# Optimization experiments

Measured on AMD Instinct MI355X. Metric: run time of the kernel, lower is better.

Reference implementation:

```python
import jax, jax.numpy as jnp
import numpy as np

N, NFEAT, NHID, NCLASS, NLAYERS = 4096, 512, 512, 40, 3
NEG = -9e15


def _adj(key, p=0.01):
    # sparse binary adjacency with self-loops, matching the `adj > 0` masking
    a = (jax.random.uniform(key, (N, N)) < p).astype(jnp.float32)
    return jnp.minimum(a + jnp.eye(N, dtype=jnp.float32), 1.0)


def setup_inputs() -> dict:
    key = jax.random.key(0)
    ks = jax.random.split(key, 16)
    inp = {
        "x": jax.random.normal(ks[0], (N, NFEAT), jnp.float32),
        "adj_att": _adj(ks[1]),
        "adj1": _adj(ks[2]),
        "adj2": _adj(ks[3]),
        "hop_select": jnp.ones((NLAYERS,), jnp.float32),
    }
    s1 = 1.0 / np.sqrt(NFEAT)
    s2 = 1.0 / np.sqrt(NHID)
    for i in range(NLAYERS):
        inp[f"W_fc{i}"] = jax.random.uniform(ks[4 + i], (NFEAT, NHID), jnp.float32, -s1, s1)
        inp[f"b_fc{i}"] = jnp.zeros((NHID,), jnp.float32)
    for i in range(NLAYERS - 1):
        inp[f"W_q{i}"] = jax.random.uniform(ks[7 + 2 * i], (NHID, NHID), jnp.float32, -s2, s2)
        inp[f"b_q{i}"] = jnp.zeros((NHID,), jnp.float32)
        inp[f"W_k{i}"] = jax.random.uniform(ks[8 + 2 * i], (NHID, NHID), jnp.float32, -s2, s2)
        inp[f"b_k{i}"] = jnp.zeros((NHID,), jnp.float32)
    s3 = 1.0 / np.sqrt(NHID * NLAYERS)
    inp["W_cls"] = jax.random.uniform(ks[11], (NHID * NLAYERS, NCLASS), jnp.float32, -s3, s3)
    inp["b_cls"] = jnp.zeros((NCLASS,), jnp.float32)
    return inp


def _gatv3_forward(x, adj_att, adj1, adj2, hop_select,
                   W_fc0, b_fc0, W_fc1, b_fc1, W_fc2, b_fc2,
                   W_q0, b_q0, W_k0, b_k0, W_q1, b_q1, W_k1, b_k1,
                   W_cls, b_cls):
    mask = jax.nn.softmax(hop_select, axis=-1)
    adjs = [None, adj1, adj2]
    fc = [(W_fc0, b_fc0), (W_fc1, b_fc1), (W_fc2, b_fc2)]
    qk = [(W_q0, b_q0, W_k0, b_k0), (W_q1, b_q1, W_k1, b_k1)]
    outs = []
    tmp_1 = None
    for i in range(NLAYERS):
        W, b = fc[i]
        tmp = x @ W + b  # [N, nhid]
        if adjs[i] is not None:
            adj = adjs[i]
            Wq, bq, Wk, bk = qk[i - 1]
            t_att = adj_att @ tmp                      # [N, nhid]
            Q = adj_att @ (t_att @ Wq + bq)            # GCN1 Q, act=None
            K = adj_att @ (t_att @ Wk + bk)            # GCN1 K, act=None
            scores = jnp.where(adj > 0, Q @ K.T, NEG)  # masked QK^T
            att = jax.nn.softmax(scores, axis=-1)
            tmp_1 = jnp.where(adj > 0, att, 0.0)
            tmp = att @ tmp
        # F.normalize(p=2, dim=1) with eps=1e-12 clamp
        nrm = jnp.maximum(jnp.sqrt(jnp.sum(tmp * tmp, axis=1, keepdims=True)), 1e-12)
        outs.append(mask[i] * (tmp / nrm))
    final = jnp.concatenate(outs, axis=1)          # [N, 3*nhid]
    out = jax.nn.relu(final)                       # dropout is identity in eval
    logits = out @ W_cls + b_cls
    return jax.nn.log_softmax(logits, axis=1), tmp_1


def reference(x, adj_att, adj1, adj2, hop_select,
              W_fc0, b_fc0, W_fc1, b_fc1, W_fc2, b_fc2,
              W_q0, b_q0, W_k0, b_k0, W_q1, b_q1, W_k1, b_k1,
              W_cls, b_cls):
    return _gatv3_forward(x, adj_att, adj1, adj2, hop_select,
                          W_fc0, b_fc0, W_fc1, b_fc1, W_fc2, b_fc2,
                          W_q0, b_q0, W_k0, b_k0, W_q1, b_q1, W_k1, b_k1,
                          W_cls, b_cls)
```

## Files before the change

kernel.cpp:

```cpp
#include <hip/hip_runtime.h>
#include <math.h>

#define NN 4096
#define DD 512
#define ELL 128

typedef unsigned long long u64;
typedef __attribute__((ext_vector_type(8))) short short8;
typedef __attribute__((ext_vector_type(8))) unsigned short ushort8;
typedef __attribute__((ext_vector_type(4))) float f32x4;

static __device__ __forceinline__ unsigned short f2bf(float f) {
  unsigned u = __float_as_uint(f);
  unsigned r = (u + 0x7fffu + ((u >> 16) & 1u)) >> 16;
  return (unsigned short)r;
}
static __device__ __forceinline__ float bf2f(unsigned short h) {
  return __uint_as_float(((unsigned)h) << 16);
}

struct Build3 {
  const float *adj0, *adj1, *adj2;
  int *c0, *c1, *c2;
  int *n0, *n1, *n2;
};

__global__ __launch_bounds__(256) void k_build3(Build3 p) {
  const int s = blockIdx.y;
  const float* adj = s == 0 ? p.adj0 : (s == 1 ? p.adj1 : p.adj2);
  int* cols = s == 0 ? p.c0 : (s == 1 ? p.c1 : p.c2);
  int* cnt  = s == 0 ? p.n0 : (s == 1 ? p.n1 : p.n2);
  const int wv = threadIdx.x >> 6;
  const int lane = threadIdx.x & 63;
  const int r = blockIdx.x * 4 + wv;
  const float* row = adj + (size_t)r * NN;
  int* rc = cols + (size_t)r * ELL;
  int base = 0;
  for (int c0 = 0; c0 < NN; c0 += 256) {
    float4 v = *(const float4*)(row + c0 + lane * 4);
    u64 m0 = __ballot(v.x > 0.f);
    u64 m1 = __ballot(v.y > 0.f);
    u64 m2 = __ballot(v.z > 0.f);
    u64 m3 = __ballot(v.w > 0.f);
    u64 below = (1ull << lane) - 1ull;
    int pre = base + __popcll(m0 & below) + __popcll(m1 & below) +
              __popcll(m2 & below) + __popcll(m3 & below);
    int own = 0;
    const int cb = c0 + 4 * lane;
    if (v.x > 0.f) { int id = pre + own; if (id < ELL) rc[id] = cb + 0; own++; }
    if (v.y > 0.f) { int id = pre + own; if (id < ELL) rc[id] = cb + 1; own++; }
    if (v.z > 0.f) { int id = pre + own; if (id < ELL) rc[id] = cb + 2; own++; }
    if (v.w > 0.f) { int id = pre + own; if (id < ELL) rc[id] = cb + 3; own++; }
    base += __popcll(m0) + __popcll(m1) + __popcll(m2) + __popcll(m3);
  }
  if (lane == 0) cnt[r] = base < ELL ? base : ELL;
}

struct SplitE { const float* src; unsigned short* dst; int rows; int bstyle; };
struct Split4 { SplitE e[4]; };

__global__ __launch_bounds__(256) void k_split(Split4 p) {
  SplitE e = p.e[blockIdx.y];
  if (!e.src) return;
  const int oct = blockIdx.x * 256 + threadIdx.x;
  if (oct >= e.rows * 64) return;
  float v[8];
  size_t toff;
  if (!e.bstyle) {
    const int m = oct >> 6, kg = oct & 63;
    const float* sp = e.src + (size_t)m * 512 + kg * 8;
    float4 u0 = *(const float4*)sp;
    float4 u1 = *(const float4*)(sp + 4);
    v[0] = u0.x; v[1] = u0.y; v[2] = u0.z; v[3] = u0.w;
    v[4] = u1.x; v[5] = u1.y; v[6] = u1.z; v[7] = u1.w;
    toff = ((size_t)(m >> 7) * 16 + (kg >> 2)) * 4096 +
           (size_t)((m & 127) >> 4) * 512 + (size_t)(kg & 3) * 128 +
           (size_t)(m & 15) * 8;
  } else {
    const int n = oct & 511, kog = oct >> 9;
    const int k0 = kog * 8;
#pragma unroll
    for (int i = 0; i < 8; i++) v[i] = e.src[(size_t)(k0 + i) * 512 + n];
    toff = ((size_t)(n >> 7) * 16 + (kog >> 2)) * 4096 +
           (size_t)((n & 127) >> 4) * 512 + (size_t)(kog & 3) * 128 +
           (size_t)(n & 15) * 8;
  }
  ushort8 h0, h1, h2;
#pragma unroll
  for (int i = 0; i < 8; i++) {
    float f = v[i];
    unsigned short a0 = f2bf(f);
    float r1 = f - bf2f(a0);
    unsigned short a1 = f2bf(r1);
    float r2 = r1 - bf2f(a1);
    unsigned short a2 = f2bf(r2);
    h0[i] = a0; h1[i] = a1; h2[i] = a2;
  }
  const size_t stride = (size_t)e.rows * 512;
  *(ushort8*)(e.dst + toff) = h0;
  *(ushort8*)(e.dst + stride + toff) = h1;
  *(ushort8*)(e.dst + 2 * stride + toff) = h2;
}

struct ToBf {
  const float *s0, *s1;
  unsigned short *d0, *d1;
};

__global__ __launch_bounds__(256) void k_tobf16(ToBf p) {
  const float* s = blockIdx.y ? p.s1 : p.s0;
  unsigned short* d = blockIdx.y ? p.d1 : p.d0;
  const size_t i = ((size_t)blockIdx.x * 256 + threadIdx.x) * 8;
  float4 a = *(const float4*)(s + i);
  float4 b = *(const float4*)(s + i + 4);
  ushort8 h;
  h[0] = f2bf(a.x); h[1] = f2bf(a.y); h[2] = f2bf(a.z); h[3] = f2bf(a.w);
  h[4] = f2bf(b.x); h[5] = f2bf(b.y); h[6] = f2bf(b.z); h[7] = f2bf(b.w);
  *(ushort8*)(d + i) = h;
}

struct GmP {
  const unsigned short *A0, *A1, *A2;
  const unsigned short *B0, *B1, *B2;
  const float *b0, *b1, *b2;
  float *C0, *C1, *C2;
  size_t sA, sB;
};

#define MMTERM(sa)                                                          \
  _Pragma("unroll")                                                         \
  for (int mi = 0; mi < 4; mi++) {                                          \
    _Pragma("unroll")                                                       \
    for (int ni = 0; ni < 4; ni++)                                          \
      acc[mi][ni] = __builtin_amdgcn_mfma_f32_16x16x32_bf16(                \
          af[sa][mi], bf[ni], acc[mi][ni], 0, 0, 0);                        \
  }

__global__ __launch_bounds__(256) void k_gemm_mfma(GmP p) {
  __shared__ __align__(16) unsigned short Al[3][4096];
  __shared__ __align__(16) unsigned short Bl[3][4096];
  const int tid = threadIdx.x;
  const int mat = blockIdx.y >> 2;
  const int nb = blockIdx.y & 3;
  const int mb = blockIdx.x;
  const unsigned short* A = mat == 0 ? p.A0 : (mat == 1 ? p.A1 : p.A2);
  const unsigned short* B = mat == 0 ? p.B0 : (mat == 1 ? p.B1 : p.B2);
  const float* bias = mat == 0 ? p.b0 : (mat == 1 ? p.b1 : p.b2);
  float* C = mat == 0 ? p.C0 : (mat == 1 ? p.C1 : p.C2);
  const int lane = tid & 63, w = tid >> 6, wr = w >> 1, wc = w & 1;
  const size_t s8A = p.sA >> 3, s8B = p.sB >> 3;

  f32x4 acc[4][4];
#pragma unroll
  for (int mi = 0; mi < 4; mi++)
#pragma unroll
    for (int ni = 0; ni < 4; ni++) acc[mi][ni] = (f32x4){0.f, 0.f, 0.f, 0.f};

  for (int kb = 0; kb < 16; kb++) {
    const short8* ga = (const short8*)(A + ((size_t)mb * 16 + kb) * 4096);
    const short8* gb = (const short8*)(B + ((size_t)nb * 16 + kb) * 4096);
    __syncthreads();
#pragma unroll
    for (int s = 0; s < 3; s++) {
#pragma unroll
      for (int c = 0; c < 2; c++) {
        const int o = tid + c * 256;
        ((short8*)Al[s])[o] = ga[(size_t)s * s8A + o];
        ((short8*)Bl[s])[o] = gb[(size_t)s * s8B + o];
      }
    }
    __syncthreads();
    short8 af[3][4];
#pragma unroll
    for (int s = 0; s < 3; s++)
#pragma unroll
      for (int mi = 0; mi < 4; mi++)
        af[s][mi] = ((const short8*)Al[s])[(wr * 4 + mi) * 64 + lane];
    short8 bf[4];
#pragma unroll
    for (int ni = 0; ni < 4; ni++)
      bf[ni] = ((const short8*)Bl[0])[(wc * 4 + ni) * 64 + lane];
    MMTERM(0) MMTERM(1) MMTERM(2)
#pragma unroll
    for (int ni = 0; ni < 4; ni++)
      bf[ni] = ((const short8*)Bl[1])[(wc * 4 + ni) * 64 + lane];
    MMTERM(0) MMTERM(1)
#pragma unroll
    for (int ni = 0; ni < 4; ni++)
      bf[ni] = ((const short8*)Bl[2])[(wc * 4 + ni) * 64 + lane];
    MMTERM(0)
  }

  const int m0 = mb * 128 + wr * 64;
  const int n0c = nb * 128 + wc * 64 + (lane & 15);
  const int r0 = (lane >> 4) * 4;
#pragma unroll
  for (int mi = 0; mi < 4; mi++) {
#pragma unroll
    for (int ni = 0; ni < 4; ni++) {
      const int col = n0c + ni * 16;
      const float bb = bias ? bias[col] : 0.f;
      f32x4 a = acc[mi][ni];
#pragma unroll
      for (int r = 0; r < 4; r++)
        C[(size_t)(m0 + mi * 16 + r0 + r) * DD + col] = a[r] + bb;
    }
  }
}

struct GemmNT {
  const float *A0, *B0, *A1, *B1;
  float *C0, *C1;
};

__global__ __launch_bounds__(256) void k_gemm_nt(GemmNT p) {
  __shared__ __align__(16) float As[32][68];
  __shared__ __align__(16) float Bs[32][68];
  const int tid = threadIdx.x;
  const int mat = blockIdx.y >> 3;
  const int n0 = (blockIdx.y & 7) * 64;
  const int m0 = blockIdx.x * 64;
  const float* A = mat == 0 ? p.A0 : p.A1;
  const float* B = mat == 0 ? p.B0 : p.B1;
  float* C       = mat == 0 ? p.C0 : p.C1;
  const int tx = tid & 15, ty = tid >> 4;
  const int lr = tid >> 3, lc = (tid & 7) * 4;

  float4 fa[2], fb[2];
#pragma unroll
  for (int q = 0; q < 2; q++) {
    fa[q] = *(const float4*)(A + (size_t)(m0 + lr + 32 * q) * DD + lc);
    fb[q] = *(const float4*)(B + (size_t)(n0 + lr + 32 * q) * DD + lc);
  }
#pragma unroll
  for (int q = 0; q < 2; q++) {
    As[lc + 0][lr + 32 * q] = fa[q].x;
    As[lc + 1][lr + 32 * q] = fa[q].y;
    As[lc + 2][lr + 32 * q] = fa[q].z;
    As[lc + 3][lr + 32 * q] = fa[q].w;
    Bs[lc + 0][lr + 32 * q] = fb[q].x;
    Bs[lc + 1][lr + 32 * q] = fb[q].y;
    Bs[lc + 2][lr + 32 * q] = fb[q].z;
    Bs[lc + 3][lr + 32 * q] = fb[q].w;
  }
  __syncthreads();

  float acc[4][4];
#pragma unroll
  for (int i = 0; i < 4; i++)
#pragma unroll
    for (int j = 0; j < 4; j++) acc[i][j] = 0.f;

  for (int t = 0; t < 16; t++) {
    if (t < 15) {
      const int k0 = (t + 1) * 32;
#pragma unroll
      for (int q = 0; q < 2; q++) {
        fa[q] = *(const float4*)(A + (size_t)(m0 + lr + 32 * q) * DD + k0 + lc);
        fb[q] = *(const float4*)(B + (size_t)(n0 + lr + 32 * q) * DD + k0 + lc);
      }
    }
#pragma unroll
    for (int kk = 0; kk < 32; kk++) {
      float4 a = *(const float4*)&As[kk][ty * 4];
      float4 b = *(const float4*)&Bs[kk][tx * 4];
      float av[4] = {a.x, a.y, a.z, a.w};
      float bv[4] = {b.x, b.y, b.z, b.w};
#pragma unroll
      for (int i = 0; i < 4; i++)
#pragma unroll
        for (int j = 0; j < 4; j++) acc[i][j] = fmaf(av[i], bv[j], acc[i][j]);
    }
    __syncthreads();
    if (t < 15) {
#pragma unroll
      for (int q = 0; q < 2; q++) {
        As[lc + 0][lr + 32 * q] = fa[q].x;
        As[lc + 1][lr + 32 * q] = fa[q].y;
        As[lc + 2][lr + 32 * q] = fa[q].z;
        As[lc + 3][lr + 32 * q] = fa[q].w;
        Bs[lc + 0][lr + 32 * q] = fb[q].x;
        Bs[lc + 1][lr + 32 * q] = fb[q].y;
        Bs[lc + 2][lr + 32 * q] = fb[q].z;
        Bs[lc + 3][lr + 32 * q] = fb[q].w;
      }
      __syncthreads();
    }
  }

#pragma unroll
  for (int i = 0; i < 4; i++) {
    const int m = m0 + ty * 4 + i;
    float4 o = {acc[i][0], acc[i][1], acc[i][2], acc[i][3]};
    *(float4*)(C + (size_t)m * DD + n0 + tx * 4) = o;
  }
}

struct W12P {
  const float *Wq0, *bk0, *Wk0, *bq0;
  const float *Wq1, *bk1, *Wk1, *bq1;
  float *w10, *w20, *w11, *w21, *gam;
};

__global__ __launch_bounds__(256) void k_w12(W12P p) {
  const int l = blockIdx.y;
  const float* Wq = l ? p.Wq1 : p.Wq0;
  const float* bk = l ? p.bk1 : p.bk0;
  const float* Wk = l ? p.Wk1 : p.Wk0;
  const float* bq = l ? p.bq1 : p.bq0;
  float* w1 = l ? p.w11 : p.w10;
  float* w2 = l ? p.w21 : p.w20;
  const int wv = threadIdx.x >> 6, lane = threadIdx.x & 63;
  const int r = blockIdx.x * 4 + wv;
  float s1 = 0.f, s2 = 0.f;
  for (int k = lane; k < DD; k += 64) {
    s1 = fmaf(Wq[(size_t)r * DD + k], bk[k], s1);
    s2 = fmaf(Wk[(size_t)r * DD + k], bq[k], s2);
  }
#pragma unroll
  for (int off = 32; off > 0; off >>= 1) {
    s1 += __shfl_xor(s1, off);
    s2 += __shfl_xor(s2, off);
  }
  if (lane == 0) { w1[r] = s1; w2[r] = s2; }
  if (blockIdx.x == 0 && wv == 0) {
    float g = 0.f;
    for (int k = lane; k < DD; k += 64) g = fmaf(bq[k], bk[k], g);
#pragma unroll
    for (int off = 32; off > 0; off >>= 1) g += __shfl_xor(g, off);
    if (lane == 0) p.gam[l] = g;
  }
}

struct AbP {
  const float *U1, *U2, *w10, *w20, *w11, *w21;
  float *a1, *b1, *a2, *b2;
};

__global__ __launch_bounds__(256) void k_ab(AbP p) {
  const int wv = threadIdx.x >> 6, lane = threadIdx.x & 63;
  const int r = blockIdx.x * 4 + wv;
  const int base = lane * 8;
  float4 wa0 = *(const float4*)(p.w10 + base);
  float4 wa1 = *(const float4*)(p.w10 + base + 4);
  float4 wb0 = *(const float4*)(p.w20 + base);
  float4 wb1 = *(const float4*)(p.w20 + base + 4);
  float4 u0 = *(const float4*)(p.U1 + (size_t)r * DD + base);
  float4 u1 = *(const float4*)(p.U1 + (size_t)r * DD + base + 4);
  float sa = u0.x * wa0.x + u0.y * wa0.y + u0.z * wa0.z + u0.w * wa0.w +
             u1.x * wa1.x + u1.y * wa1.y + u1.z * wa1.z + u1.w * wa1.w;
  float sb = u0.x * wb0.x + u0.y * wb0.y + u0.z * wb0.z + u0.w * wb0.w +
             u1.x * wb1.x + u1.y * wb1.y + u1.z * wb1.z + u1.w * wb1.w;
#pragma unroll
  for (int off = 32; off > 0; off >>= 1) {
    sa += __shfl_xor(sa, off);
    sb += __shfl_xor(sb, off);
  }
  if (lane == 0) { p.a1[r] = sa; p.b1[r] = sb; }
  wa0 = *(const float4*)(p.w11 + base);
  wa1 = *(const float4*)(p.w11 + base + 4);
  wb0 = *(const float4*)(p.w21 + base);
  wb1 = *(const float4*)(p.w21 + base + 4);
  u0 = *(const float4*)(p.U2 + (size_t)r * DD + base);
  u1 = *(const float4*)(p.U2 + (size_t)r * DD + base + 4);
  sa = u0.x * wa0.x + u0.y * wa0.y + u0.z * wa0.z + u0.w * wa0.w +
       u1.x * wa1.x + u1.y * wa1.y + u1.z * wa1.z + u1.w * wa1.w;
  sb = u0.x * wb0.x + u0.y * wb0.y + u0.z * wb0.z + u0.w * wb0.w +
       u1.x * wb1.x + u1.y * wb1.y + u1.z * wb1.z + u1.w * wb1.w;
#pragma unroll
  for (int off = 32; off > 0; off >>= 1) {
    sa += __shfl_xor(sa, off);
    sb += __shfl_xor(sb, off);
  }
  if (lane == 0) { p.a2[r] = sa; p.b2[r] = sb; }
}

struct Sd2 {
  const int *cols0, *cnts0, *cols1, *cnts1;
  const float *V0, *U0, *al0, *be0;
  const unsigned short *T0;
  const float *V1, *U1, *al1, *be1;
  const unsigned short *T1;
  const float* gam;
  const int* degA;
  float *out0, *out1, *dense;
};

__global__ __launch_bounds__(256) void k_sddmm_out(Sd2 p) {
  const int l = blockIdx.y;
  const int* cols = l ? p.cols1 : p.cols0;
  const int* cnts = l ? p.cnts1 : p.cnts0;
  const float* V = l ? p.V1 : p.V0;
  const float* U = l ? p.U1 : p.U0;
  const float* al = l ? p.al1 : p.al0;
  const float* be = l ? p.be1 : p.be0;
  const unsigned short* Tb = l ? p.T1 : p.T0;
  float* out = l ? p.out1 : p.out0;
  float* dense = l ? p.dense : nullptr;
  const int r = blockIdx.x;
  const int t = threadIdx.x;
  const int lane = t & 63, wv = t >> 6;
  const int cnt = cnts[r];
  __shared__ int scol[ELL];
  __shared__ float ssc[ELL];
  if (t < ELL) scol[t] = (t < cnt) ? cols[(size_t)r * ELL + t] : 0;
  if (dense) {
    float4 z = {0.f, 0.f, 0.f, 0.f};
    float4* drow = (float4*)(dense + (size_t)r * NN);
#pragma unroll
    for (int q = 0; q < 4; q++) drow[t + 256 * q] = z;
  }
  __syncthreads();
  const float g = p.gam[l];
  const float dr = (float)p.degA[r];
  const float ar = al[r];
  const float* Vr = V + (size_t)r * DD + lane * 8;
  float4 q0 = *(const float4*)Vr;
  float4 q1 = *(const float4*)(Vr + 4);
  for (int k = wv; k < cnt; k += 4) {
    const int c = scol[k];
    const float* Uc = U + (size_t)c * DD + lane * 8;
    float4 k0 = *(const float4*)Uc;
    float4 k1 = *(const float4*)(Uc + 4);
    float s = q0.x * k0.x + q0.y * k0.y + q0.z * k0.z + q0.w * k0.w +
              q1.x * k1.x + q1.y * k1.y + q1.z * k1.z + q1.w * k1.w;
#pragma unroll
    for (int off = 32; off > 0; off >>= 1) s += __shfl_xor(s, off);
    if (lane == 0) {
      const float dc = (float)p.degA[c];
      ssc[k] = s + dc * ar + dr * be[c] + dr * dc * g;
    }
  }
  __syncthreads();
  if (wv == 0) {
    float v0 = (lane < cnt) ? ssc[lane] : -INFINITY;
    float v1 = (lane + 64 < cnt) ? ssc[lane + 64] : -INFINITY;
    float mx = fmaxf(v0, v1);
#pragma unroll
    for (int off = 32; off > 0; off >>= 1) mx = fmaxf(mx, __shfl_xor(mx, off));
    float e0 = (lane < cnt) ? expf(v0 - mx) : 0.f;
    float e1 = (lane + 64 < cnt) ? expf(v1 - mx) : 0.f;
    float sm = e0 + e1;
#pragma unroll
    for (int off = 32; off > 0; off >>= 1) sm += __shfl_xor(sm, off);
    float inv = 1.f / sm;
    if (lane < cnt) ssc[lane] = e0 * inv;
    if (lane + 64 < cnt) ssc[lane + 64] = e1 * inv;
  }
  __syncthreads();
  if (t < cnt && dense) dense[(size_t)r * NN + scol[t]] = ssc[t];
  float a0 = 0.f, a1 = 0.f;
#pragma unroll 4
  for (int k = 0; k < cnt; k++) {
    const float v = ssc[k];
    const unsigned u = *(const unsigned*)(Tb + (size_t)scol[k] * DD + t * 2);
    a0 = fmaf(v, __uint_as_float(u << 16), a0);
    a1 = fmaf(v, __uint_as_float(u & 0xffff0000u), a1);
  }
  float2 o = {a0, a1};
  *(float2*)(out + (size_t)r * DD + t * 2) = o;
}

struct SpF {
  const int *colsA, *cntsA, *colsB, *cntsB;
  const float *BA, *BB;
  float *CA, *CB;
};

__global__ __launch_bounds__(256) void k_spmm_f4(SpF p) {
  const int mat = blockIdx.y;
  const int* cols = mat ? p.colsB : p.colsA;
  const int* cnts = mat ? p.cntsB : p.cntsA;
  const float* B = mat ? p.BB : p.BA;
  float* C = mat ? p.CB : p.CA;
  const int hr = threadIdx.x >> 7;
  const int j = threadIdx.x & 127;
  const int row = blockIdx.x * 2 + hr;
  __shared__ int scol[2][ELL];
  const int cnt = cnts[row];
  scol[hr][j] = (j < cnt) ? cols[(size_t)row * ELL + j] : 0;
  __syncthreads();
  float4 acc = {0.f, 0.f, 0.f, 0.f};
#pragma unroll 4
  for (int k = 0; k < cnt; k++) {
    float4 b = *(const float4*)(B + (size_t)scol[hr][k] * DD + j * 4);
    acc.x += b.x; acc.y += b.y; acc.z += b.z; acc.w += b.w;
  }
  *(float4*)(C + (size_t)row * DD + j * 4) = acc;
}

__global__ __launch_bounds__(256) void k_norm_cls(const float* __restrict__ T0,
                                                  const float* __restrict__ T1,
                                                  const float* __restrict__ T2,
                                                  const float* __restrict__ hop,
                                                  const float* __restrict__ Wc,
                                                  const float* __restrict__ bc,
                                                  float* __restrict__ out) {
  const int r = blockIdx.x;
  const int t = threadIdx.x;
  const int lane = t & 63, wv = t >> 6;
  __shared__ __align__(16) float srow[1536];
  __shared__ float red[4];
  __shared__ float pr[6][40];
  float h0 = hop[0], h1 = hop[1], h2 = hop[2];
  float hm = fmaxf(h0, fmaxf(h1, h2));
  float e0 = expf(h0 - hm), e1 = expf(h1 - hm), e2 = expf(h2 - hm);
  float minv = 1.f / (e0 + e1 + e2);
  float mask[3] = {e0 * minv, e1 * minv, e2 * minv};
  const float* Ts[3] = {T0, T1, T2};
#pragma unroll
  for (int s = 0; s < 3; s++) {
    float x0 = Ts[s][(size_t)r * DD + t];
    float x1 = Ts[s][(size_t)r * DD + t + 256];
    float ss = x0 * x0 + x1 * x1;
#pragma unroll
    for (int off = 32; off > 0; off >>= 1) ss += __shfl_xor(ss, off);
    if (lane == 0) red[wv] = ss;
    __syncthreads();
    float tot = red[0] + red[1] + red[2] + red[3];
    float nrm = fmaxf(sqrtf(tot), 1e-12f);
    float sc = mask[s] / nrm;
    srow[s * DD + t] = fmaxf(x0 * sc, 0.f);
    srow[s * DD + t + 256] = fmaxf(x1 * sc, 0.f);
    __syncthreads();
  }
  float part = 0.f;
  const int col = t % 40, seg = t / 40;
  if (seg < 6) {
    const float* w = Wc + col;
#pragma unroll 4
    for (int k = seg * 256; k < seg * 256 + 256; k++)
      part = fmaf(srow[k], w[(size_t)k * 40], part);
    pr[seg][col] = part;
  }
  __syncthreads();
  if (t < 64) {
    float lg = -INFINITY;
    if (t < 40) {
      lg = bc[t];
#pragma unroll
      for (int s6 = 0; s6 < 6; s6++) lg += pr[s6][t];
    }
    float mx = lg;
#pragma unroll
    for (int off = 32; off > 0; off >>= 1) mx = fmaxf(mx, __shfl_xor(mx, off));
    float ex = (t < 40) ? expf(lg - mx) : 0.f;
    float sm = ex;
#pragma unroll
    for (int off = 32; off > 0; off >>= 1) sm += __shfl_xor(sm, off);
    float ls = logf(sm);
    if (t < 40) out[(size_t)r * 40 + t] = lg - mx - ls;
  }
}

extern "C" void kernel_launch(void* const* d_in, const int* in_sizes, int n_in,
                              void* d_out, int out_size, void* d_ws, size_t ws_size,
                              hipStream_t stream) {
  (void)in_sizes; (void)n_in; (void)out_size; (void)ws_size;
  const float* x    = (const float*)d_in[0];
  const float* adjA = (const float*)d_in[1];
  const float* adj1 = (const float*)d_in[2];
  const float* adj2 = (const float*)d_in[3];
  const float* hop  = (const float*)d_in[4];
  const float* Wfc0 = (const float*)d_in[5];  const float* bfc0 = (const float*)d_in[6];
  const float* Wfc1 = (const float*)d_in[7];  const float* bfc1 = (const float*)d_in[8];
  const float* Wfc2 = (const float*)d_in[9];  const float* bfc2 = (const float*)d_in[10];
  const float* Wq0  = (const float*)d_in[11]; const float* bq0  = (const float*)d_in[12];
  const float* Wk0  = (const float*)d_in[13]; const float* bk0  = (const float*)d_in[14];
  const float* Wq1  = (const float*)d_in[15]; const float* bq1  = (const float*)d_in[16];
  const float* Wk1  = (const float*)d_in[17]; const float* bk1  = (const float*)d_in[18];
  const float* Wc   = (const float*)d_in[19]; const float* bc   = (const float*)d_in[20];

  float* ws = (float*)d_ws;
  const size_t MD = (size_t)NN * DD;
  const size_t WD = (size_t)DD * DD;
  float* TMP0 = ws + 0 * MD;
  float* TMP1 = ws + 1 * MD;
  float* TMP2 = ws + 2 * MD;
  float* S3   = ws + 3 * MD;
  float* S4   = ws + 4 * MD;
  float* U1   = ws + 5 * MD;
  float* U2   = ws + 6 * MD;
  float* M1   = ws + 7 * MD;
  float* M2   = M1 + WD;
  float* w10 = M2 + WD;
  float* w20 = w10 + DD;
  float* w11 = w20 + DD;
  float* w21 = w11 + DD;
  float* gam = w21 + DD;
  float* AL1 = gam + 4;
  float* BE1 = AL1 + NN;
  float* AL2 = BE1 + NN;
  float* BE2 = AL2 + NN;
  int* ELLA = (int*)(BE2 + NN);
  int* ELL1 = ELLA + (size_t)NN * ELL;
  int* ELL2 = ELL1 + (size_t)NN * ELL;
  int* CNTA = ELL2 + (size_t)NN * ELL;
  int* CNT1 = CNTA + NN;
  int* CNT2 = CNT1 + NN;
  unsigned short* Tb1 = (unsigned short*)(CNT2 + NN);
  unsigned short* Tb2 = Tb1 + MD;

  float* outLog = (float*)d_out;
  float* outAtt = outLog + (size_t)NN * 40;
  unsigned short* xb   = (unsigned short*)outAtt;
  unsigned short* wfcb = xb + 3 * MD;
  unsigned short* Ub1  = wfcb + 9 * WD;
  unsigned short* Ub2  = Ub1 + 3 * MD;
  unsigned short* Mb1  = Ub2 + 3 * MD;
  unsigned short* Mb2  = Mb1 + 3 * WD;

  Build3 pb{adjA, adj1, adj2, ELLA, ELL1, ELL2, CNTA, CNT1, CNT2};
  k_build3<<<dim3(NN / 4, 3), 256, 0, stream>>>(pb);

  W12P pw{Wq0, bk0, Wk0, bq0, Wq1, bk1, Wk1, bq1, w10, w20, w11, w21, gam};
  k_w12<<<dim3(DD / 4, 2), 256, 0, stream>>>(pw);

  Split4 sp1{{{x, xb, NN, 0},
              {Wfc0, wfcb + 0 * 3 * WD, DD, 1},
              {Wfc1, wfcb + 1 * 3 * WD, DD, 1},
              {Wfc2, wfcb + 2 * 3 * WD, DD, 1}}};
  k_split<<<dim3(1024, 4), 256, 0, stream>>>(sp1);

  GmP pf{xb, xb, xb,
         wfcb + 0 * 3 * WD, wfcb + 1 * 3 * WD, wfcb + 2 * 3 * WD,
         bfc0, bfc1, bfc2, TMP0, TMP1, TMP2, MD, WD};
  k_gemm_mfma<<<dim3(32, 12), 256, 0, stream>>>(pf);

  GemmNT pm{Wq0, Wk0, Wq1, Wk1, M1, M2};
  k_gemm_nt<<<dim3(8, 16), 256, 0, stream>>>(pm);

  ToBf tb{TMP1, TMP2, Tb1, Tb2};
  k_tobf16<<<dim3(1024, 2), 256, 0, stream>>>(tb);

  SpF s1{ELLA, CNTA, ELLA, CNTA, TMP1, TMP2, S3, S4};
  k_spmm_f4<<<dim3(NN / 2, 2), 256, 0, stream>>>(s1);
  SpF s2{ELLA, CNTA, ELLA, CNTA, S3, S4, U1, U2};
  k_spmm_f4<<<dim3(NN / 2, 2), 256, 0, stream>>>(s2);

  Split4 sp2{{{U1, Ub1, NN, 0},
              {U2, Ub2, NN, 0},
              {M1, Mb1, DD, 1},
              {M2, Mb2, DD, 1}}};
  k_split<<<dim3(1024, 4), 256, 0, stream>>>(sp2);

  GmP pv{Ub1, Ub2, nullptr, Mb1, Mb2, nullptr,
         nullptr, nullptr, nullptr, S3, S4, nullptr, MD, WD};
  k_gemm_mfma<<<dim3(32, 8), 256, 0, stream>>>(pv);

  AbP pab{U1, U2, w10, w20, w11, w21, AL1, BE1, AL2, BE2};
  k_ab<<<NN / 4, 256, 0, stream>>>(pab);

  Sd2 sd{ELL1, CNT1, ELL2, CNT2,
         S3, U1, AL1, BE1, Tb1,
         S4, U2, AL2, BE2, Tb2,
         gam, CNTA, S3, S4, outAtt};
  k_sddmm_out<<<dim3(NN, 2), 256, 0, stream>>>(sd);

  k_norm_cls<<<NN, 256, 0, stream>>>(TMP0, S3, S4, hop, Wc, bc, outLog);
}
```

Baseline: 439.1 us.

## Split fused SDDMM-softmax-PV kernel into score and PV kernels

The fused sparse attention kernel is split into two kernels. The first computes masked scores and softmax and writes the attention values to an ELL buffer and to the dense output. The second does the sparse attention-times-values product with two rows per block and four bf16 columns per thread, using 8-byte loads in place of 4-byte ones. This shortens the serial score phase, improves load width in the gather loop, and lets the out arrays S3/S4 be read and written safely across kernels. The cost is an extra launch plus a round trip of the attention values through global memory, and it reuses the TMP1/TMP2 buffers as scratch.

```diff
diff --git a/kernel.cpp b/kernel.cpp
--- a/kernel.cpp
+++ b/kernel.cpp
@@ -375,18 +375,16 @@
   if (lane == 0) { p.a2[r] = sa; p.b2[r] = sb; }
 }
 
-struct Sd2 {
+struct ScP {
   const int *cols0, *cnts0, *cols1, *cnts1;
   const float *V0, *U0, *al0, *be0;
-  const unsigned short *T0;
   const float *V1, *U1, *al1, *be1;
-  const unsigned short *T1;
   const float* gam;
   const int* degA;
-  float *out0, *out1, *dense;
-};
-
-__global__ __launch_bounds__(256) void k_sddmm_out(Sd2 p) {
+  float *av0, *av1, *dense;
+};
+
+__global__ __launch_bounds__(256) void k_score(ScP p) {
   const int l = blockIdx.y;
   const int* cols = l ? p.cols1 : p.cols0;
   const int* cnts = l ? p.cnts1 : p.cnts0;
@@ -394,8 +392,7 @@
   const float* U = l ? p.U1 : p.U0;
   const float* al = l ? p.al1 : p.al0;
   const float* be = l ? p.be1 : p.be0;
-  const unsigned short* Tb = l ? p.T1 : p.T0;
-  float* out = l ? p.out1 : p.out0;
+  float* av = l ? p.av1 : p.av0;
   float* dense = l ? p.dense : nullptr;
   const int r = blockIdx.x;
   const int t = threadIdx.x;
@@ -448,17 +445,48 @@
     if (lane + 64 < cnt) ssc[lane + 64] = e1 * inv;
   }
   __syncthreads();
-  if (t < cnt && dense) dense[(size_t)r * NN + scol[t]] = ssc[t];
-  float a0 = 0.f, a1 = 0.f;
+  if (t < cnt) {
+    const float v = ssc[t];
+    av[(size_t)r * ELL + t] = v;
+    if (dense) dense[(size_t)r * NN + scol[t]] = v;
+  }
+}
+
+struct PvP {
+  const int *cols0, *cnts0, *cols1, *cnts1;
+  const float *av0, *av1;
+  const unsigned short *T0, *T1;
+  float *out0, *out1;
+};
+
+__global__ __launch_bounds__(256) void k_pv(PvP p) {
+  const int l = blockIdx.y;
+  const int* cols = l ? p.cols1 : p.cols0;
+  const int* cnts = l ? p.cnts1 : p.cnts0;
+  const float* av = l ? p.av1 : p.av0;
+  const unsigned short* Tb = l ? p.T1 : p.T0;
+  float* out = l ? p.out1 : p.out0;
+  const int hr = threadIdx.x >> 7;
+  const int j = threadIdx.x & 127;
+  const int row = blockIdx.x * 2 + hr;
+  __shared__ int scol[2][ELL];
+  __shared__ float sval[2][ELL];
+  const int cnt = cnts[row];
+  scol[hr][j] = (j < cnt) ? cols[(size_t)row * ELL + j] : 0;
+  sval[hr][j] = (j < cnt) ? av[(size_t)row * ELL + j] : 0.f;
+  __syncthreads();
+  float a0 = 0.f, a1 = 0.f, a2 = 0.f, a3 = 0.f;
 #pragma unroll 4
   for (int k = 0; k < cnt; k++) {
-    const float v = ssc[k];
-    const unsigned u = *(const unsigned*)(Tb + (size_t)scol[k] * DD + t * 2);
-    a0 = fmaf(v, __uint_as_float(u << 16), a0);
-    a1 = fmaf(v, __uint_as_float(u & 0xffff0000u), a1);
-  }
-  float2 o = {a0, a1};
-  *(float2*)(out + (size_t)r * DD + t * 2) = o;
+    const float v = sval[hr][k];
+    const uint2 u = *(const uint2*)(Tb + (size_t)scol[hr][k] * DD + j * 4);
+    a0 = fmaf(v, __uint_as_float(u.x << 16), a0);
+    a1 = fmaf(v, __uint_as_float(u.x & 0xffff0000u), a1);
+    a2 = fmaf(v, __uint_as_float(u.y << 16), a2);
+    a3 = fmaf(v, __uint_as_float(u.y & 0xffff0000u), a3);
+  }
+  float4 o = {a0, a1, a2, a3};
+  *(float4*)(out + (size_t)row * DD + j * 4) = o;
 }
 
 struct SpF {
@@ -600,6 +628,8 @@
   int* CNT2 = CNT1 + NN;
   unsigned short* Tb1 = (unsigned short*)(CNT2 + NN);
   unsigned short* Tb2 = Tb1 + MD;
+  float* ATTV1 = TMP1;
+  float* ATTV2 = TMP2;
 
   float* outLog = (float*)d_out;
   float* outAtt = outLog + (size_t)NN * 40;
@@ -651,11 +681,14 @@
   AbP pab{U1, U2, w10, w20, w11, w21, AL1, BE1, AL2, BE2};
   k_ab<<<NN / 4, 256, 0, stream>>>(pab);
 
-  Sd2 sd{ELL1, CNT1, ELL2, CNT2,
-         S3, U1, AL1, BE1, Tb1,
-         S4, U2, AL2, BE2, Tb2,
-         gam, CNTA, S3, S4, outAtt};
-  k_sddmm_out<<<dim3(NN, 2), 256, 0, stream>>>(sd);
+  ScP sc{ELL1, CNT1, ELL2, CNT2,
+         S3, U1, AL1, BE1,
+         S4, U2, AL2, BE2,
+         gam, CNTA, ATTV1, ATTV2, outAtt};
+  k_score<<<dim3(NN, 2), 256, 0, stream>>>(sc);
+
+  PvP pp{ELL1, CNT1, ELL2, CNT2, ATTV1, ATTV2, Tb1, Tb2, S3, S4};
+  k_pv<<<dim3(NN / 2, 2), 256, 0, stream>>>(pp);
 
   k_norm_cls<<<NN, 256, 0, stream>>>(TMP0, S3, S4, hop, Wc, bc, outLog);
 }
```

New measurement: 430.5 us. About the same (-2.0%).
